# Performance work log

Hardware: AMD Instinct MI355X
Metric: run time of the kernel (lower is better)

## Reference

```python
import jax, jax.numpy as jnp
import numpy as np

B, T, H, L = 64, 512, 768, 9


def _crf_logZ(logits, transitions, seqlen):
    # forward algorithm; state freezes at t >= seqlen (tfa semantics)
    Tn = logits.shape[1]
    alpha0 = logits[:, 0]  # [B,L]
    valid = (jnp.arange(1, Tn)[None, :] < seqlen[:, None]).T  # [T-1,B]
    xs = (jnp.swapaxes(logits[:, 1:], 0, 1), valid)

    def step(alpha, inp):
        logit_t, v = inp
        new = jax.nn.logsumexp(alpha[:, :, None] + transitions[None], axis=1) + logit_t
        return jnp.where(v[:, None], new, alpha), None

    alphaT, _ = jax.lax.scan(step, alpha0, xs)
    return jax.nn.logsumexp(alphaT, axis=1)  # [B]


def _crf_score(logits, transitions, label, seqlen):
    Tn = logits.shape[1]
    seqmask = (jnp.arange(Tn)[None, :] < seqlen[:, None]).astype(logits.dtype)  # [B,T]
    unary = jnp.take_along_axis(logits, label[..., None], axis=2)[..., 0]
    unary = jnp.sum(unary * seqmask, axis=1)
    trans = transitions[label[:, :-1], label[:, 1:]]
    trans = jnp.sum(trans * seqmask[:, 1:], axis=1)
    return unary + trans  # [B]


def _viterbi(logits, transitions, seqlen):
    Tn, Ln = logits.shape[1], logits.shape[2]
    alpha0 = logits[:, 0]
    valid = (jnp.arange(1, Tn)[None, :] < seqlen[:, None]).T  # [T-1,B]
    xs = (jnp.swapaxes(logits[:, 1:], 0, 1), valid)
    idL = jnp.arange(Ln, dtype=jnp.int32)

    def step(alpha, inp):
        logit_t, v = inp
        scores = alpha[:, :, None] + transitions[None]  # [B,L,L]
        new = jnp.max(scores, axis=1) + logit_t
        bp = jnp.argmax(scores, axis=1).astype(jnp.int32)  # [B,L]
        alpha = jnp.where(v[:, None], new, alpha)
        bp = jnp.where(v[:, None], bp, idL[None, :])  # identity bp on padded steps
        return alpha, bp

    alphaT, bps = jax.lax.scan(step, alpha0, xs)  # bps: [T-1,B,L]
    last = jnp.argmax(alphaT, axis=1).astype(jnp.int32)  # [B]

    def back(tag, bp):
        prev = jnp.take_along_axis(bp, tag[:, None], axis=1)[:, 0]
        return prev, tag

    first, rest = jax.lax.scan(back, last, bps, reverse=True)
    tags = jnp.concatenate([first[None], rest], axis=0)  # [T,B]
    return jnp.swapaxes(tags, 0, 1)  # [B,T]


def setup_inputs() -> dict:
    key = jax.random.key(0)
    k = jax.random.split(key, 6)
    x = jax.random.normal(k[0], (B, T, H), dtype=jnp.float32)
    W = jax.random.truncated_normal(k[1], -2.0, 2.0, (H, L), dtype=jnp.float32) * 0.02
    b = jnp.zeros((L,), dtype=jnp.float32)
    lim = float(np.sqrt(6.0 / (L + L)))  # glorot_uniform
    transitions = jax.random.uniform(k[2], (L, L), dtype=jnp.float32, minval=-lim, maxval=lim)
    label = jax.random.randint(k[3], (B, T), 0, L, dtype=jnp.int32)
    seqlen = jax.random.randint(k[4], (B,), 1, T + 1, dtype=jnp.int32)
    mask = jnp.arange(T)[None, :] < seqlen[:, None]
    return {"x": x, "W": W, "b": b, "transitions": transitions, "label": label, "seqlen": seqlen, "mask": mask}


def reference(x, W, b, transitions, label, seqlen, mask):
    logits = jnp.einsum('bth,hl->btl', x, W) + b  # dense_ner
    ll = _crf_score(logits, transitions, label, seqlen) - _crf_logZ(logits, transitions, seqlen)
    loss = jnp.mean(-ll)
    vit = _viterbi(logits, transitions, seqlen)
    seqmask = (jnp.arange(logits.shape[1])[None, :] < seqlen[:, None]).astype(jnp.float32)
    accuracy = jnp.sum((vit == label).astype(jnp.float32) * seqmask) / jnp.sum(seqlen.astype(jnp.float32))
    tp = jnp.sum(((label > 0) & (vit == label)).astype(jnp.float32))
    tn = jnp.sum(((label > 0) & (vit != label)).astype(jnp.float32))
    fp = jnp.sum((mask & (label == 0) & (vit > 0)).astype(jnp.float32))
    return vit, tp, tn, fp, loss, accuracy
```

## Files before the change

### kernel.cpp

```cpp
#include <hip/hip_runtime.h>
#include <stdint.h>
#include <math.h>

#define NB 64
#define BT 512
#define NH 768
#define NL 9
#define PBT 528
#define PADW 772

__device__ __forceinline__ float rlane(float v, int i) {
    return __int_as_float(__builtin_amdgcn_readlane(__float_as_int(v), i));
}

template<int CTRL, int RM>
__device__ __forceinline__ float dppadd(float v) {
    const int t = __builtin_amdgcn_update_dpp(0, __float_as_int(v), CTRL, RM, 0xf, true);
    return v + __int_as_float(t);
}

__device__ __forceinline__ float wave_sum_dpp(float v) {
    v = dppadd<0x111, 0xf>(v);
    v = dppadd<0x112, 0xf>(v);
    v = dppadd<0x114, 0xf>(v);
    v = dppadd<0x118, 0xf>(v);
    v = dppadd<0x142, 0xa>(v);
    v = dppadd<0x143, 0xc>(v);
    return rlane(v, 63);
}

__global__ __launch_bounds__(256, 2) void gemm_kernel(
    const float* __restrict__ x, const float* __restrict__ W,
    const float* __restrict__ bias, float* __restrict__ logits)
{
    __shared__ float wT[NL * PADW];

    const int tid  = threadIdx.x;
    const int lane = tid & 63;

    for (int i = tid; i < NH * NL; i += 256) {
        const int h = i / NL, l = i - h * NL;
        wT[l * PADW + h] = W[i];
    }
    __syncthreads();

    float wr[3][NL][4];
#pragma unroll
    for (int k = 0; k < 3; ++k)
#pragma unroll
        for (int l = 0; l < NL; ++l) {
            const float4 w4 = *(const float4*)&wT[l * PADW + k * 256 + lane * 4];
            wr[k][l][0] = w4.x; wr[k][l][1] = w4.y;
            wr[k][l][2] = w4.z; wr[k][l][3] = w4.w;
        }
    const float bj = bias[lane < NL ? lane : 0];

    const int gwave = (blockIdx.x * blockDim.x + tid) >> 6;
    const int nw    = (gridDim.x * blockDim.x) >> 6;
    const int nrows = NB * BT;
    int row = gwave;
    if (row >= nrows) return;

    const float4* xr = (const float4*)(x + (size_t)row * NH);
    float4 a0 = xr[lane], a1 = xr[64 + lane], a2 = xr[128 + lane];

    while (true) {
        const int nrow = row + nw;
        float4 b0, b1, b2;
        if (nrow < nrows) {
            const float4* xn = (const float4*)(x + (size_t)nrow * NH);
            b0 = xn[lane]; b1 = xn[64 + lane]; b2 = xn[128 + lane];
        }

        float acc[NL];
#pragma unroll
        for (int l = 0; l < NL; ++l) {
            float s = a0.x * wr[0][l][0];
            s = fmaf(a0.y, wr[0][l][1], s);
            s = fmaf(a0.z, wr[0][l][2], s);
            s = fmaf(a0.w, wr[0][l][3], s);
            s = fmaf(a1.x, wr[1][l][0], s);
            s = fmaf(a1.y, wr[1][l][1], s);
            s = fmaf(a1.z, wr[1][l][2], s);
            s = fmaf(a1.w, wr[1][l][3], s);
            s = fmaf(a2.x, wr[2][l][0], s);
            s = fmaf(a2.y, wr[2][l][1], s);
            s = fmaf(a2.z, wr[2][l][2], s);
            s = fmaf(a2.w, wr[2][l][3], s);
            acc[l] = s;
        }
        float sum[NL];
#pragma unroll
        for (int l = 0; l < NL; ++l) sum[l] = wave_sum_dpp(acc[l]);
        float outv = sum[0];
#pragma unroll
        for (int l = 1; l < NL; ++l) outv = (lane == l) ? sum[l] : outv;
        if (lane < NL) logits[(size_t)row * NL + lane] = outv + bj;

        row = nrow;
        if (row >= nrows) break;
        a0 = b0; a1 = b1; a2 = b2;
    }
}

__global__ __launch_bounds__(256) void crf_kernel(
    const float* __restrict__ logits, const float* __restrict__ trans,
    const int* __restrict__ label, const int* __restrict__ seqlen,
    float* __restrict__ vit_out, float* __restrict__ stats)
{
    __shared__ __align__(16) float lg_lds[PBT * NL];
    __shared__ float    val_lds[BT * NL];
    __shared__ float    trans_lds[NL * NL];
    __shared__ uint8_t  bp_lds[(BT - 1) * NL];
    __shared__ uint64_t packed_lds[BT - 1];
    __shared__ uint8_t  vit_lds[BT];
    __shared__ float    xw[4][4];

    const int b    = blockIdx.x;
    const int tid  = threadIdx.x;
    const int lane = tid & 63;
    const int wv   = tid >> 6;
    const int sl   = seqlen[b];
    const float* lg  = logits + (size_t)b * BT * NL;
    const int*   lab = label + (size_t)b * BT;

    {
        const float4* src = (const float4*)lg;
        float4* dst = (float4*)lg_lds;
        for (int idx = tid; idx < BT * NL / 4; idx += 256) dst[idx] = src[idx];
        for (int idx = BT * NL + tid; idx < PBT * NL; idx += 256) lg_lds[idx] = 0.f;
        if (tid < NL * NL) trans_lds[tid] = trans[tid];
    }
    __syncthreads();

    if (wv == 0) {
        const int j = lane < NL ? lane : 0;
        float E[NL];
#pragma unroll
        for (int i = 0; i < NL; ++i) E[i] = __expf(trans_lds[i * NL + j]) * 0.125f;
        float A = __expf(lg_lds[j]);
        int lc = 0;
        for (int tb = 1; tb < BT + 8; tb += 8) {
            float P[8];
#pragma unroll
            for (int s = 0; s < 8; ++s) P[s] = __expf(lg_lds[(tb + s) * NL + j]);
#pragma unroll
            for (int s = 0; s < 8; ++s) {
                const int t = tb + s;
                const float r0 = rlane(A, 0), r1 = rlane(A, 1), r2 = rlane(A, 2),
                            r3 = rlane(A, 3), r4 = rlane(A, 4), r5 = rlane(A, 5),
                            r6 = rlane(A, 6), r7 = rlane(A, 7), r8 = rlane(A, 8);
                float p0 = r0 * E[0]; p0 = fmaf(r1, E[1], p0); p0 = fmaf(r2, E[2], p0);
                float p1 = r3 * E[3]; p1 = fmaf(r4, E[4], p1); p1 = fmaf(r5, E[5], p1);
                float p2 = r6 * E[6]; p2 = fmaf(r7, E[7], p2); p2 = fmaf(r8, E[8], p2);
                const float An = ((p0 + p1) + p2) * P[s];
                A = (t < sl) ? An : A;
            }
            const float m = fmaxf(fmaxf(
                fmaxf(fmaxf(rlane(A, 0), rlane(A, 1)), fmaxf(rlane(A, 2), rlane(A, 3))),
                fmaxf(fmaxf(rlane(A, 4), rlane(A, 5)), fmaxf(rlane(A, 6), rlane(A, 7)))),
                rlane(A, 8));
            const int ex = (int)((__float_as_uint(m) >> 23) & 0xFFu) - 126;
            const float sc = __uint_as_float((uint32_t)(127 - ex) << 23);
            A *= sc;
            lc += ex;
        }
        const float sum = ((rlane(A, 0) + rlane(A, 1)) + (rlane(A, 2) + rlane(A, 3))) +
                          ((rlane(A, 4) + rlane(A, 5)) + (rlane(A, 6) + rlane(A, 7))) +
                          rlane(A, 8);
        const float logZ = logf(sum) +
            ((float)lc + 3.0f * (float)(sl - 1)) * 0.6931471805599453f;
        if (lane == 0) stats[b * 8 + 1] = logZ;
    } else if (wv == 1) {
        const int j = lane < NL ? lane : 0;
        float tc[NL];
#pragma unroll
        for (int i = 0; i < NL; ++i) tc[i] = trans_lds[i * NL + j];
        float v = lg_lds[j];
        if (lane < NL) val_lds[j] = v;
        for (int tb = 1; tb < BT + 8; tb += 8) {
            float lv[8];
#pragma unroll
            for (int s = 0; s < 8; ++s) lv[s] = lg_lds[(tb + s) * NL + j];
#pragma unroll
            for (int s = 0; s < 8; ++s) {
                const int t = tb + s;
                const float r0 = rlane(v, 0), r1 = rlane(v, 1), r2 = rlane(v, 2),
                            r3 = rlane(v, 3), r4 = rlane(v, 4), r5 = rlane(v, 5),
                            r6 = rlane(v, 6), r7 = rlane(v, 7), r8 = rlane(v, 8);
                const float c0 = r0 + tc[0], c1 = r1 + tc[1], c2 = r2 + tc[2],
                            c3 = r3 + tc[3], c4 = r4 + tc[4], c5 = r5 + tc[5],
                            c6 = r6 + tc[6], c7 = r7 + tc[7], c8 = r8 + tc[8];
                const float m = fmaxf(fmaxf(fmaxf(fmaxf(c0, c1), c2),
                                            fmaxf(fmaxf(c3, c4), c5)),
                                      fmaxf(fmaxf(c6, c7), c8));
                const float nv = m + lv[s];
                v = (t < sl) ? nv : v;
                if (lane < NL && t < BT) val_lds[t * NL + lane] = v;
            }
        }
        const float r0 = rlane(v, 0), r1 = rlane(v, 1), r2 = rlane(v, 2),
                    r3 = rlane(v, 3), r4 = rlane(v, 4), r5 = rlane(v, 5),
                    r6 = rlane(v, 6), r7 = rlane(v, 7), r8 = rlane(v, 8);
        const float m = fmaxf(fmaxf(fmaxf(fmaxf(r0, r1), r2),
                                    fmaxf(fmaxf(r3, r4), r5)),
                              fmaxf(fmaxf(r6, r7), r8));
        const int last = (r0 == m) ? 0 : (r1 == m) ? 1 : (r2 == m) ? 2 :
                         (r3 == m) ? 3 : (r4 == m) ? 4 : (r5 == m) ? 5 :
                         (r6 == m) ? 6 : (r7 == m) ? 7 : 8;
        if (lane == 0) vit_lds[BT - 1] = (uint8_t)last;
    } else if (wv == 2) {
        float s = 0.f;
        for (int t = lane; t < BT; t += 64) {
            const int lb = lab[t];
            if (t < sl) {
                s += lg_lds[t * NL + lb];
                if (t >= 1) s += trans_lds[lab[t - 1] * NL + lb];
            }
        }
#pragma unroll
        for (int off = 32; off >= 1; off >>= 1) s += __shfl_xor(s, off, 64);
        if (lane == 0) stats[b * 8 + 0] = s;
    }
    __syncthreads();

    for (int idx = tid; idx < (BT - 1) * NL; idx += 256) {
        const int tm1 = idx / NL;
        const int jj  = idx - tm1 * NL;
        const int t   = tm1 + 1;
        int bi;
        if (t >= sl) bi = jj;
        else {
            float best = val_lds[tm1 * NL] + trans_lds[jj];
            bi = 0;
#pragma unroll
            for (int i = 1; i < NL; ++i) {
                const float c = val_lds[tm1 * NL + i] + trans_lds[i * NL + jj];
                if (c > best) { best = c; bi = i; }
            }
        }
        bp_lds[idx] = (uint8_t)bi;
    }
    __syncthreads();

    for (int r = tid; r < BT - 1; r += 256) {
        uint64_t p = 0;
#pragma unroll
        for (int i = 0; i < NL; ++i)
            p |= (uint64_t)bp_lds[r * NL + i] << (4 * i);
        packed_lds[r] = p;
    }
    __syncthreads();

    if (tid == 0) {
        int tag = vit_lds[BT - 1];
        for (int t = BT - 2; t >= 0; --t) {
            const uint64_t row = packed_lds[t];
            tag = (int)((row >> (4 * tag)) & 15u);
            vit_lds[t] = (uint8_t)tag;
        }
    }
    __syncthreads();

    float accv = 0.f, tpv = 0.f, tnv = 0.f, fpv = 0.f;
    for (int t = tid; t < BT; t += 256) {
        const int tg = vit_lds[t];
        const int lb = lab[t];
        const bool msk = t < sl;
        vit_out[(size_t)b * BT + t] = (float)tg;
        if (msk && tg == lb) accv += 1.f;
        if (lb > 0 && tg == lb) tpv += 1.f;
        if (lb > 0 && tg != lb) tnv += 1.f;
        if (msk && lb == 0 && tg > 0) fpv += 1.f;
    }
#pragma unroll
    for (int off = 32; off >= 1; off >>= 1) {
        accv += __shfl_xor(accv, off, 64);
        tpv  += __shfl_xor(tpv,  off, 64);
        tnv  += __shfl_xor(tnv,  off, 64);
        fpv  += __shfl_xor(fpv,  off, 64);
    }
    if (lane == 0) { xw[0][wv] = accv; xw[1][wv] = tpv; xw[2][wv] = tnv; xw[3][wv] = fpv; }
    __syncthreads();
    if (tid == 0) {
        stats[b * 8 + 2] = xw[0][0] + xw[0][1] + xw[0][2] + xw[0][3];
        stats[b * 8 + 3] = xw[1][0] + xw[1][1] + xw[1][2] + xw[1][3];
        stats[b * 8 + 4] = xw[2][0] + xw[2][1] + xw[2][2] + xw[2][3];
        stats[b * 8 + 5] = xw[3][0] + xw[3][1] + xw[3][2] + xw[3][3];
    }
}

__global__ __launch_bounds__(64) void finalize_kernel(
    const float* __restrict__ stats, const int* __restrict__ seqlen,
    float* __restrict__ out)
{
    const int lane = threadIdx.x;
    float score = stats[lane * 8 + 0];
    float logZ  = stats[lane * 8 + 1];
    float accv  = stats[lane * 8 + 2];
    float tpv   = stats[lane * 8 + 3];
    float tnv   = stats[lane * 8 + 4];
    float fpv   = stats[lane * 8 + 5];
    float nll   = logZ - score;
    float slf   = (float)seqlen[lane];
#pragma unroll
    for (int off = 32; off >= 1; off >>= 1) {
        nll  += __shfl_xor(nll,  off, 64);
        accv += __shfl_xor(accv, off, 64);
        tpv  += __shfl_xor(tpv,  off, 64);
        tnv  += __shfl_xor(tnv,  off, 64);
        fpv  += __shfl_xor(fpv,  off, 64);
        slf  += __shfl_xor(slf,  off, 64);
    }
    if (lane == 0) {
        out[NB * BT + 0] = tpv;
        out[NB * BT + 1] = tnv;
        out[NB * BT + 2] = fpv;
        out[NB * BT + 3] = nll / (float)NB;
        out[NB * BT + 4] = accv / slf;
    }
}

extern "C" void kernel_launch(void* const* d_in, const int* in_sizes, int n_in,
                              void* d_out, int out_size, void* d_ws, size_t ws_size,
                              hipStream_t stream)
{
    const float* x      = (const float*)d_in[0];
    const float* W      = (const float*)d_in[1];
    const float* bias   = (const float*)d_in[2];
    const float* trans  = (const float*)d_in[3];
    const int*   label  = (const int*)d_in[4];
    const int*   seqlen = (const int*)d_in[5];

    float* out    = (float*)d_out;
    float* logits = (float*)d_ws;
    float* stats  = logits + (size_t)NB * BT * NL;

    gemm_kernel<<<512, 256, 0, stream>>>(x, W, bias, logits);
    crf_kernel<<<NB, 256, 0, stream>>>(logits, trans, label, seqlen, out, stats);
    finalize_kernel<<<1, 64, 0, stream>>>(stats, seqlen, out);
}
```

Measured before the change: 212.7 us.

## Pack 8 sequences per CRF block, fuse Viterbi backpointers into forward scan

The CRF kernel now runs 8 batch rows per 1024-thread block. Waves 0-7 run the forward logZ recursion and later a wave-parallel backtrace that uses readlane over packed backpointers. Waves 8-15 run Viterbi, computing the argmax backpointers inline so the separate backpointer pass and the val_lds buffer are no longer needed. Logits are read straight from global memory with one-block-ahead register prefetch instead of being staged in LDS, and the GEMM prefetches two rows ahead. The CRF launch drops to 8 blocks, which gives fewer CUs in exchange for lower per-sequence overhead. The score computation moves onto the waves that also do Viterbi.

```diff
diff --git a/kernel.cpp b/kernel.cpp
--- a/kernel.cpp
+++ b/kernel.cpp
@@ -6,11 +6,15 @@
 #define BT 512
 #define NH 768
 #define NL 9
-#define PBT 528
 #define PADW 772
+#define BPB 8
+#define BPROW 16
 
 __device__ __forceinline__ float rlane(float v, int i) {
     return __int_as_float(__builtin_amdgcn_readlane(__float_as_int(v), i));
+}
+__device__ __forceinline__ uint32_t rlane_u(uint32_t v, int i) {
+    return (uint32_t)__builtin_amdgcn_readlane((int)v, i);
 }
 
 template<int CTRL, int RM>
@@ -64,12 +68,19 @@
     const float4* xr = (const float4*)(x + (size_t)row * NH);
     float4 a0 = xr[lane], a1 = xr[64 + lane], a2 = xr[128 + lane];
 
+    int r1 = row + nw;
+    float4 b0{}, b1{}, b2{};
+    if (r1 < nrows) {
+        const float4* xn = (const float4*)(x + (size_t)r1 * NH);
+        b0 = xn[lane]; b1 = xn[64 + lane]; b2 = xn[128 + lane];
+    }
+
     while (true) {
-        const int nrow = row + nw;
-        float4 b0, b1, b2;
-        if (nrow < nrows) {
-            const float4* xn = (const float4*)(x + (size_t)nrow * NH);
-            b0 = xn[lane]; b1 = xn[64 + lane]; b2 = xn[128 + lane];
+        const int r2 = r1 + nw;
+        float4 c0{}, c1{}, c2{};
+        if (r2 < nrows) {
+            const float4* xn = (const float4*)(x + (size_t)r2 * NH);
+            c0 = xn[lane]; c1 = xn[64 + lane]; c2 = xn[128 + lane];
         }
 
         float acc[NL];
@@ -97,53 +108,50 @@
         for (int l = 1; l < NL; ++l) outv = (lane == l) ? sum[l] : outv;
         if (lane < NL) logits[(size_t)row * NL + lane] = outv + bj;
 
-        row = nrow;
-        if (row >= nrows) break;
+        if (r1 >= nrows) break;
         a0 = b0; a1 = b1; a2 = b2;
-    }
-}
-
-__global__ __launch_bounds__(256) void crf_kernel(
+        b0 = c0; b1 = c1; b2 = c2;
+        row = r1; r1 = r2;
+    }
+}
+
+__global__ __launch_bounds__(1024) void crf_kernel(
     const float* __restrict__ logits, const float* __restrict__ trans,
     const int* __restrict__ label, const int* __restrict__ seqlen,
     float* __restrict__ vit_out, float* __restrict__ stats)
 {
-    __shared__ __align__(16) float lg_lds[PBT * NL];
-    __shared__ float    val_lds[BT * NL];
-    __shared__ float    trans_lds[NL * NL];
-    __shared__ uint8_t  bp_lds[(BT - 1) * NL];
-    __shared__ uint64_t packed_lds[BT - 1];
-    __shared__ uint8_t  vit_lds[BT];
-    __shared__ float    xw[4][4];
-
-    const int b    = blockIdx.x;
+    __shared__ uint8_t  bp_lds[BPB * (BT - 1) * BPROW];
+    __shared__ uint64_t packed_lds[BPB * (BT - 1)];
+    __shared__ uint8_t  vit_lds[BPB * BT];
+
     const int tid  = threadIdx.x;
     const int lane = tid & 63;
     const int wv   = tid >> 6;
+    const int w    = wv & 7;
+    const int b    = blockIdx.x * BPB + w;
     const int sl   = seqlen[b];
     const float* lg  = logits + (size_t)b * BT * NL;
     const int*   lab = label + (size_t)b * BT;
-
-    {
-        const float4* src = (const float4*)lg;
-        float4* dst = (float4*)lg_lds;
-        for (int idx = tid; idx < BT * NL / 4; idx += 256) dst[idx] = src[idx];
-        for (int idx = BT * NL + tid; idx < PBT * NL; idx += 256) lg_lds[idx] = 0.f;
-        if (tid < NL * NL) trans_lds[tid] = trans[tid];
-    }
-    __syncthreads();
-
-    if (wv == 0) {
-        const int j = lane < NL ? lane : 0;
+    const int j = lane < NL ? lane : 0;
+
+    if (wv < 8) {
         float E[NL];
 #pragma unroll
-        for (int i = 0; i < NL; ++i) E[i] = __expf(trans_lds[i * NL + j]) * 0.125f;
-        float A = __expf(lg_lds[j]);
+        for (int i = 0; i < NL; ++i) E[i] = __expf(trans[i * NL + j]) * 0.125f;
+        float A = __expf(lg[j]);
         int lc = 0;
+        float cur[8], nxt[8];
+#pragma unroll
+        for (int s = 0; s < 8; ++s) cur[s] = lg[(1 + s) * NL + j];
         for (int tb = 1; tb < BT + 8; tb += 8) {
+#pragma unroll
+            for (int s = 0; s < 8; ++s) {
+                int tt = tb + 8 + s; if (tt > BT - 1) tt = BT - 1;
+                nxt[s] = lg[tt * NL + j];
+            }
             float P[8];
 #pragma unroll
-            for (int s = 0; s < 8; ++s) P[s] = __expf(lg_lds[(tb + s) * NL + j]);
+            for (int s = 0; s < 8; ++s) P[s] = __expf(cur[s]);
 #pragma unroll
             for (int s = 0; s < 8; ++s) {
                 const int t = tb + s;
@@ -156,14 +164,16 @@
                 const float An = ((p0 + p1) + p2) * P[s];
                 A = (t < sl) ? An : A;
             }
-            const float m = fmaxf(fmaxf(
-                fmaxf(fmaxf(rlane(A, 0), rlane(A, 1)), fmaxf(rlane(A, 2), rlane(A, 3))),
-                fmaxf(fmaxf(rlane(A, 4), rlane(A, 5)), fmaxf(rlane(A, 6), rlane(A, 7)))),
-                rlane(A, 8));
+            const float m = fmaxf(
+                fmaxf(fmaxf(fmaxf(rlane(A, 0), rlane(A, 1)), rlane(A, 2)),
+                      fmaxf(fmaxf(rlane(A, 3), rlane(A, 4)), rlane(A, 5))),
+                fmaxf(fmaxf(rlane(A, 6), rlane(A, 7)), rlane(A, 8)));
             const int ex = (int)((__float_as_uint(m) >> 23) & 0xFFu) - 126;
             const float sc = __uint_as_float((uint32_t)(127 - ex) << 23);
             A *= sc;
             lc += ex;
+#pragma unroll
+            for (int s = 0; s < 8; ++s) cur[s] = nxt[s];
         }
         const float sum = ((rlane(A, 0) + rlane(A, 1)) + (rlane(A, 2) + rlane(A, 3))) +
                           ((rlane(A, 4) + rlane(A, 5)) + (rlane(A, 6) + rlane(A, 7))) +
@@ -171,17 +181,20 @@
         const float logZ = logf(sum) +
             ((float)lc + 3.0f * (float)(sl - 1)) * 0.6931471805599453f;
         if (lane == 0) stats[b * 8 + 1] = logZ;
-    } else if (wv == 1) {
-        const int j = lane < NL ? lane : 0;
+    } else {
         float tc[NL];
 #pragma unroll
-        for (int i = 0; i < NL; ++i) tc[i] = trans_lds[i * NL + j];
-        float v = lg_lds[j];
-        if (lane < NL) val_lds[j] = v;
+        for (int i = 0; i < NL; ++i) tc[i] = trans[i * NL + j];
+        float v = lg[j];
+        float cur[8], nxt[8];
+#pragma unroll
+        for (int s = 0; s < 8; ++s) cur[s] = lg[(1 + s) * NL + j];
         for (int tb = 1; tb < BT + 8; tb += 8) {
-            float lv[8];
-#pragma unroll
-            for (int s = 0; s < 8; ++s) lv[s] = lg_lds[(tb + s) * NL + j];
+#pragma unroll
+            for (int s = 0; s < 8; ++s) {
+                int tt = tb + 8 + s; if (tt > BT - 1) tt = BT - 1;
+                nxt[s] = lg[tt * NL + j];
+            }
 #pragma unroll
             for (int s = 0; s < 8; ++s) {
                 const int t = tb + s;
@@ -191,31 +204,84 @@
                 const float c0 = r0 + tc[0], c1 = r1 + tc[1], c2 = r2 + tc[2],
                             c3 = r3 + tc[3], c4 = r4 + tc[4], c5 = r5 + tc[5],
                             c6 = r6 + tc[6], c7 = r7 + tc[7], c8 = r8 + tc[8];
-                const float m = fmaxf(fmaxf(fmaxf(fmaxf(c0, c1), c2),
-                                            fmaxf(fmaxf(c3, c4), c5)),
-                                      fmaxf(fmaxf(c6, c7), c8));
-                const float nv = m + lv[s];
+                const float m = fmaxf(
+                    fmaxf(fmaxf(fmaxf(c0, c1), c2), fmaxf(fmaxf(c3, c4), c5)),
+                    fmaxf(fmaxf(c6, c7), c8));
+                const float nv = m + cur[s];
                 v = (t < sl) ? nv : v;
-                if (lane < NL && t < BT) val_lds[t * NL + lane] = v;
-            }
+                int bi = 8;
+                bi = (c7 == m) ? 7 : bi;
+                bi = (c6 == m) ? 6 : bi;
+                bi = (c5 == m) ? 5 : bi;
+                bi = (c4 == m) ? 4 : bi;
+                bi = (c3 == m) ? 3 : bi;
+                bi = (c2 == m) ? 2 : bi;
+                bi = (c1 == m) ? 1 : bi;
+                bi = (c0 == m) ? 0 : bi;
+                bi = (t < sl) ? bi : j;
+                if (lane < NL && t < BT)
+                    bp_lds[(w * (BT - 1) + (t - 1)) * BPROW + lane] = (uint8_t)bi;
+            }
+#pragma unroll
+            for (int s = 0; s < 8; ++s) cur[s] = nxt[s];
         }
         const float r0 = rlane(v, 0), r1 = rlane(v, 1), r2 = rlane(v, 2),
                     r3 = rlane(v, 3), r4 = rlane(v, 4), r5 = rlane(v, 5),
                     r6 = rlane(v, 6), r7 = rlane(v, 7), r8 = rlane(v, 8);
-        const float m = fmaxf(fmaxf(fmaxf(fmaxf(r0, r1), r2),
-                                    fmaxf(fmaxf(r3, r4), r5)),
-                              fmaxf(fmaxf(r6, r7), r8));
+        const float m = fmaxf(
+            fmaxf(fmaxf(fmaxf(r0, r1), r2), fmaxf(fmaxf(r3, r4), r5)),
+            fmaxf(fmaxf(r6, r7), r8));
         const int last = (r0 == m) ? 0 : (r1 == m) ? 1 : (r2 == m) ? 2 :
                          (r3 == m) ? 3 : (r4 == m) ? 4 : (r5 == m) ? 5 :
                          (r6 == m) ? 6 : (r7 == m) ? 7 : 8;
-        if (lane == 0) vit_lds[BT - 1] = (uint8_t)last;
-    } else if (wv == 2) {
+        if (lane == 0) vit_lds[w * BT + BT - 1] = (uint8_t)last;
+    }
+    __syncthreads();
+
+    for (int idx = tid; idx < BPB * (BT - 1); idx += 1024) {
+        const int base = idx * BPROW;
+        uint64_t p = 0;
+#pragma unroll
+        for (int i = 0; i < NL; ++i)
+            p |= (uint64_t)bp_lds[base + i] << (4 * i);
+        packed_lds[idx] = p;
+    }
+    __syncthreads();
+
+    if (wv < 8) {
+        uint32_t plo[8], phi[8];
+#pragma unroll
+        for (int r = 0; r < 8; ++r) {
+            const int t = r * 64 + lane;
+            uint64_t val = 0;
+            if (t < BT - 1) val = packed_lds[w * (BT - 1) + t];
+            plo[r] = (uint32_t)val;
+            phi[r] = (uint32_t)(val >> 32);
+        }
+        int tag = vit_lds[w * BT + BT - 1];
+#pragma unroll
+        for (int r = 7; r >= 0; --r) {
+            const int lhi = (r == 7) ? 62 : 63;
+#pragma unroll 4
+            for (int l = lhi; l >= 0; --l) {
+                const uint32_t lo = rlane_u(plo[r], l);
+                const uint32_t hi = rlane_u(phi[r], l);
+                const uint32_t ww = (tag & 8) ? hi : lo;
+                tag = (int)((ww >> ((4 * tag) & 31)) & 15u);
+                if (lane == 0) vit_lds[w * BT + r * 64 + l] = (uint8_t)tag;
+            }
+        }
+    } else {
+        int labv[8];
+#pragma unroll
+        for (int k = 0; k < 8; ++k) labv[k] = lab[lane + 64 * k];
         float s = 0.f;
-        for (int t = lane; t < BT; t += 64) {
-            const int lb = lab[t];
+#pragma unroll
+        for (int k = 0; k < 8; ++k) {
+            const int t = lane + 64 * k;
             if (t < sl) {
-                s += lg_lds[t * NL + lb];
-                if (t >= 1) s += trans_lds[lab[t - 1] * NL + lb];
+                s += lg[t * NL + labv[k]];
+                if (t >= 1) s += trans[lab[t - 1] * NL + labv[k]];
             }
         }
 #pragma unroll
@@ -224,69 +290,33 @@
     }
     __syncthreads();
 
-    for (int idx = tid; idx < (BT - 1) * NL; idx += 256) {
-        const int tm1 = idx / NL;
-        const int jj  = idx - tm1 * NL;
-        const int t   = tm1 + 1;
-        int bi;
-        if (t >= sl) bi = jj;
-        else {
-            float best = val_lds[tm1 * NL] + trans_lds[jj];
-            bi = 0;
-#pragma unroll
-            for (int i = 1; i < NL; ++i) {
-                const float c = val_lds[tm1 * NL + i] + trans_lds[i * NL + jj];
-                if (c > best) { best = c; bi = i; }
-            }
-        }
-        bp_lds[idx] = (uint8_t)bi;
-    }
-    __syncthreads();
-
-    for (int r = tid; r < BT - 1; r += 256) {
-        uint64_t p = 0;
-#pragma unroll
-        for (int i = 0; i < NL; ++i)
-            p |= (uint64_t)bp_lds[r * NL + i] << (4 * i);
-        packed_lds[r] = p;
-    }
-    __syncthreads();
-
-    if (tid == 0) {
-        int tag = vit_lds[BT - 1];
-        for (int t = BT - 2; t >= 0; --t) {
-            const uint64_t row = packed_lds[t];
-            tag = (int)((row >> (4 * tag)) & 15u);
-            vit_lds[t] = (uint8_t)tag;
-        }
-    }
-    __syncthreads();
-
-    float accv = 0.f, tpv = 0.f, tnv = 0.f, fpv = 0.f;
-    for (int t = tid; t < BT; t += 256) {
-        const int tg = vit_lds[t];
-        const int lb = lab[t];
-        const bool msk = t < sl;
-        vit_out[(size_t)b * BT + t] = (float)tg;
-        if (msk && tg == lb) accv += 1.f;
-        if (lb > 0 && tg == lb) tpv += 1.f;
-        if (lb > 0 && tg != lb) tnv += 1.f;
-        if (msk && lb == 0 && tg > 0) fpv += 1.f;
-    }
-#pragma unroll
-    for (int off = 32; off >= 1; off >>= 1) {
-        accv += __shfl_xor(accv, off, 64);
-        tpv  += __shfl_xor(tpv,  off, 64);
-        tnv  += __shfl_xor(tnv,  off, 64);
-        fpv  += __shfl_xor(fpv,  off, 64);
-    }
-    if (lane == 0) { xw[0][wv] = accv; xw[1][wv] = tpv; xw[2][wv] = tnv; xw[3][wv] = fpv; }
-    __syncthreads();
-    if (tid == 0) {
-        stats[b * 8 + 2] = xw[0][0] + xw[0][1] + xw[0][2] + xw[0][3];
-        stats[b * 8 + 3] = xw[1][0] + xw[1][1] + xw[1][2] + xw[1][3];
-        stats[b * 8 + 4] = xw[2][0] + xw[2][1] + xw[2][2] + xw[2][3];
-        stats[b * 8 + 5] = xw[3][0] + xw[3][1] + xw[3][2] + xw[3][3];
+    if (wv < 8) {
+        float accv = 0.f, tpv = 0.f, tnv = 0.f, fpv = 0.f;
+#pragma unroll
+        for (int k = 0; k < 8; ++k) {
+            const int t = lane + 64 * k;
+            const int tg = vit_lds[w * BT + t];
+            const int lb = lab[t];
+            const bool msk = t < sl;
+            vit_out[(size_t)b * BT + t] = (float)tg;
+            if (msk && tg == lb) accv += 1.f;
+            if (lb > 0 && tg == lb) tpv += 1.f;
+            if (lb > 0 && tg != lb) tnv += 1.f;
+            if (msk && lb == 0 && tg > 0) fpv += 1.f;
+        }
+#pragma unroll
+        for (int off = 32; off >= 1; off >>= 1) {
+            accv += __shfl_xor(accv, off, 64);
+            tpv  += __shfl_xor(tpv,  off, 64);
+            tnv  += __shfl_xor(tnv,  off, 64);
+            fpv  += __shfl_xor(fpv,  off, 64);
+        }
+        if (lane == 0) {
+            stats[b * 8 + 2] = accv;
+            stats[b * 8 + 3] = tpv;
+            stats[b * 8 + 4] = tnv;
+            stats[b * 8 + 5] = fpv;
+        }
     }
 }
 
@@ -337,6 +367,6 @@
     float* stats  = logits + (size_t)NB * BT * NL;
 
     gemm_kernel<<<512, 256, 0, stream>>>(x, W, bias, logits);
-    crf_kernel<<<NB, 256, 0, stream>>>(logits, trans, label, seqlen, out, stats);
+    crf_kernel<<<NB / BPB, 1024, 0, stream>>>(logits, trans, label, seqlen, out, stats);
     finalize_kernel<<<1, 64, 0, stream>>>(stats, seqlen, out);
 }
```

Measured after the change: 336.3 us. 58.1% more time.

## Deepen gemm prefetch to four rows per stage with double buffering

Applied to the files above, without the earlier changes.

The grid-stride GEMM loop now runs a fixed schedule. Each wave handles 16 rows in four groups of four, and the next group's x loads are issued while the current group is computed. This keeps more global loads in flight per wave to hide HBM latency in a bandwidth-bound GEMV. It hardcodes 2048 waves (the launch grid must match) and raises register use; the launch_bounds minimum-blocks hint is dropped to allow that.

```diff
diff --git a/kernel.cpp b/kernel.cpp
--- a/kernel.cpp
+++ b/kernel.cpp
@@ -8,6 +8,7 @@
 #define NL 9
 #define PBT 528
 #define PADW 772
+#define NWAVE 2048
 
 __device__ __forceinline__ float rlane(float v, int i) {
     return __int_as_float(__builtin_amdgcn_readlane(__float_as_int(v), i));
@@ -29,7 +30,7 @@
     return rlane(v, 63);
 }
 
-__global__ __launch_bounds__(256, 2) void gemm_kernel(
+__global__ __launch_bounds__(256) void gemm_kernel(
     const float* __restrict__ x, const float* __restrict__ W,
     const float* __restrict__ bias, float* __restrict__ logits)
 {
@@ -55,51 +56,61 @@
         }
     const float bj = bias[lane < NL ? lane : 0];
 
-    const int gwave = (blockIdx.x * blockDim.x + tid) >> 6;
-    const int nw    = (gridDim.x * blockDim.x) >> 6;
-    const int nrows = NB * BT;
-    int row = gwave;
-    if (row >= nrows) return;
-
-    const float4* xr = (const float4*)(x + (size_t)row * NH);
-    float4 a0 = xr[lane], a1 = xr[64 + lane], a2 = xr[128 + lane];
-
-    while (true) {
-        const int nrow = row + nw;
-        float4 b0, b1, b2;
-        if (nrow < nrows) {
-            const float4* xn = (const float4*)(x + (size_t)nrow * NH);
-            b0 = xn[lane]; b1 = xn[64 + lane]; b2 = xn[128 + lane];
-        }
-
-        float acc[NL];
-#pragma unroll
-        for (int l = 0; l < NL; ++l) {
-            float s = a0.x * wr[0][l][0];
-            s = fmaf(a0.y, wr[0][l][1], s);
-            s = fmaf(a0.z, wr[0][l][2], s);
-            s = fmaf(a0.w, wr[0][l][3], s);
-            s = fmaf(a1.x, wr[1][l][0], s);
-            s = fmaf(a1.y, wr[1][l][1], s);
-            s = fmaf(a1.z, wr[1][l][2], s);
-            s = fmaf(a1.w, wr[1][l][3], s);
-            s = fmaf(a2.x, wr[2][l][0], s);
-            s = fmaf(a2.y, wr[2][l][1], s);
-            s = fmaf(a2.z, wr[2][l][2], s);
-            s = fmaf(a2.w, wr[2][l][3], s);
-            acc[l] = s;
-        }
-        float sum[NL];
-#pragma unroll
-        for (int l = 0; l < NL; ++l) sum[l] = wave_sum_dpp(acc[l]);
-        float outv = sum[0];
-#pragma unroll
-        for (int l = 1; l < NL; ++l) outv = (lane == l) ? sum[l] : outv;
-        if (lane < NL) logits[(size_t)row * NL + lane] = outv + bj;
-
-        row = nrow;
-        if (row >= nrows) break;
-        a0 = b0; a1 = b1; a2 = b2;
+    const int gw = (blockIdx.x * blockDim.x + tid) >> 6;
+
+    float4 buf[2][4][3];
+#pragma unroll
+    for (int q = 0; q < 4; ++q) {
+        const float4* p = (const float4*)(x + (size_t)(gw + q * NWAVE) * NH);
+        buf[0][q][0] = p[lane];
+        buf[0][q][1] = p[64 + lane];
+        buf[0][q][2] = p[128 + lane];
+    }
+
+#pragma unroll
+    for (int grp = 0; grp < 4; ++grp) {
+        const int cb = grp & 1, nb = cb ^ 1;
+        if (grp < 3) {
+#pragma unroll
+            for (int q = 0; q < 4; ++q) {
+                const float4* p = (const float4*)(
+                    x + (size_t)(gw + ((grp + 1) * 4 + q) * NWAVE) * NH);
+                buf[nb][q][0] = p[lane];
+                buf[nb][q][1] = p[64 + lane];
+                buf[nb][q][2] = p[128 + lane];
+            }
+        }
+#pragma unroll
+        for (int q = 0; q < 4; ++q) {
+            const float4 a0 = buf[cb][q][0];
+            const float4 a1 = buf[cb][q][1];
+            const float4 a2 = buf[cb][q][2];
+            float acc[NL];
+#pragma unroll
+            for (int l = 0; l < NL; ++l) {
+                float s = a0.x * wr[0][l][0];
+                s = fmaf(a0.y, wr[0][l][1], s);
+                s = fmaf(a0.z, wr[0][l][2], s);
+                s = fmaf(a0.w, wr[0][l][3], s);
+                s = fmaf(a1.x, wr[1][l][0], s);
+                s = fmaf(a1.y, wr[1][l][1], s);
+                s = fmaf(a1.z, wr[1][l][2], s);
+                s = fmaf(a1.w, wr[1][l][3], s);
+                s = fmaf(a2.x, wr[2][l][0], s);
+                s = fmaf(a2.y, wr[2][l][1], s);
+                s = fmaf(a2.z, wr[2][l][2], s);
+                s = fmaf(a2.w, wr[2][l][3], s);
+                acc[l] = s;
+            }
+            float sum[NL];
+#pragma unroll
+            for (int l = 0; l < NL; ++l) sum[l] = wave_sum_dpp(acc[l]);
+            float outv = sum[0];
+#pragma unroll
+            for (int l = 1; l < NL; ++l) outv = (lane == l) ? sum[l] : outv;
+            const int row = gw + (grp * 4 + q) * NWAVE;
+            if (lane < NL) logits[(size_t)row * NL + lane] = outv + bj;
+        }
     }
 }
 
```

Result: slower. 217.6 us (+2.3%).

## Process two sequences per CRF block to interleave independent recurrences

Applied to the files above, without the earlier changes.

Each CRF block now handles two batch rows, and the forward and Viterbi waves advance two independent recurrence chains in the same loop. The goal is instruction-level parallelism that hides the readlane and FMA latency of the serial dependency chain. In exchange the grid shrinks to 32 blocks, so fewer CUs are used. LDS per block roughly doubles, and the backtrace runs on two waves in parallel.

```diff
diff --git a/kernel.cpp b/kernel.cpp
--- a/kernel.cpp
+++ b/kernel.cpp
@@ -8,6 +8,7 @@
 #define NL 9
 #define PBT 528
 #define PADW 772
+#define NBB 2
 
 __device__ __forceinline__ float rlane(float v, int i) {
     return __int_as_float(__builtin_amdgcn_readlane(__float_as_int(v), i));
@@ -108,185 +109,283 @@
     const int* __restrict__ label, const int* __restrict__ seqlen,
     float* __restrict__ vit_out, float* __restrict__ stats)
 {
-    __shared__ __align__(16) float lg_lds[PBT * NL];
-    __shared__ float    val_lds[BT * NL];
+    __shared__ __align__(16) float lg_lds[NBB][PBT * NL];
+    __shared__ float    val_lds[NBB][BT * NL];
     __shared__ float    trans_lds[NL * NL];
-    __shared__ uint8_t  bp_lds[(BT - 1) * NL];
-    __shared__ uint64_t packed_lds[BT - 1];
-    __shared__ uint8_t  vit_lds[BT];
+    __shared__ uint8_t  bp_lds[NBB][(BT - 1) * NL];
+    __shared__ uint64_t packed_lds[NBB][BT - 1];
+    __shared__ uint8_t  vit_lds[NBB][BT];
     __shared__ float    xw[4][4];
 
-    const int b    = blockIdx.x;
     const int tid  = threadIdx.x;
     const int lane = tid & 63;
     const int wv   = tid >> 6;
-    const int sl   = seqlen[b];
-    const float* lg  = logits + (size_t)b * BT * NL;
-    const int*   lab = label + (size_t)b * BT;
+    const int b0   = blockIdx.x * NBB;
+    const int sl0  = seqlen[b0];
+    const int sl1  = seqlen[b0 + 1];
+    const float* lg0 = logits + (size_t)b0 * BT * NL;
+    const float* lg1 = lg0 + BT * NL;
+    const int j = lane < NL ? lane : 0;
 
     {
-        const float4* src = (const float4*)lg;
-        float4* dst = (float4*)lg_lds;
-        for (int idx = tid; idx < BT * NL / 4; idx += 256) dst[idx] = src[idx];
-        for (int idx = BT * NL + tid; idx < PBT * NL; idx += 256) lg_lds[idx] = 0.f;
+        const float4* s0 = (const float4*)lg0;
+        const float4* s1 = (const float4*)lg1;
+        float4* d0 = (float4*)&lg_lds[0][0];
+        float4* d1 = (float4*)&lg_lds[1][0];
+        for (int idx = tid; idx < BT * NL / 4; idx += 256) {
+            d0[idx] = s0[idx];
+            d1[idx] = s1[idx];
+        }
+        for (int idx = BT * NL + tid; idx < PBT * NL; idx += 256) {
+            lg_lds[0][idx] = 0.f;
+            lg_lds[1][idx] = 0.f;
+        }
         if (tid < NL * NL) trans_lds[tid] = trans[tid];
     }
     __syncthreads();
 
     if (wv == 0) {
-        const int j = lane < NL ? lane : 0;
         float E[NL];
 #pragma unroll
         for (int i = 0; i < NL; ++i) E[i] = __expf(trans_lds[i * NL + j]) * 0.125f;
-        float A = __expf(lg_lds[j]);
-        int lc = 0;
+        float A0 = __expf(lg_lds[0][j]);
+        float A1 = __expf(lg_lds[1][j]);
+        int lc0 = 0, lc1 = 0;
         for (int tb = 1; tb < BT + 8; tb += 8) {
-            float P[8];
-#pragma unroll
-            for (int s = 0; s < 8; ++s) P[s] = __expf(lg_lds[(tb + s) * NL + j]);
+            float P0[8], P1[8];
+#pragma unroll
+            for (int s = 0; s < 8; ++s) {
+                P0[s] = __expf(lg_lds[0][(tb + s) * NL + j]);
+                P1[s] = __expf(lg_lds[1][(tb + s) * NL + j]);
+            }
 #pragma unroll
             for (int s = 0; s < 8; ++s) {
                 const int t = tb + s;
-                const float r0 = rlane(A, 0), r1 = rlane(A, 1), r2 = rlane(A, 2),
-                            r3 = rlane(A, 3), r4 = rlane(A, 4), r5 = rlane(A, 5),
-                            r6 = rlane(A, 6), r7 = rlane(A, 7), r8 = rlane(A, 8);
-                float p0 = r0 * E[0]; p0 = fmaf(r1, E[1], p0); p0 = fmaf(r2, E[2], p0);
-                float p1 = r3 * E[3]; p1 = fmaf(r4, E[4], p1); p1 = fmaf(r5, E[5], p1);
-                float p2 = r6 * E[6]; p2 = fmaf(r7, E[7], p2); p2 = fmaf(r8, E[8], p2);
-                const float An = ((p0 + p1) + p2) * P[s];
-                A = (t < sl) ? An : A;
-            }
-            const float m = fmaxf(fmaxf(
-                fmaxf(fmaxf(rlane(A, 0), rlane(A, 1)), fmaxf(rlane(A, 2), rlane(A, 3))),
-                fmaxf(fmaxf(rlane(A, 4), rlane(A, 5)), fmaxf(rlane(A, 6), rlane(A, 7)))),
-                rlane(A, 8));
-            const int ex = (int)((__float_as_uint(m) >> 23) & 0xFFu) - 126;
-            const float sc = __uint_as_float((uint32_t)(127 - ex) << 23);
-            A *= sc;
-            lc += ex;
-        }
-        const float sum = ((rlane(A, 0) + rlane(A, 1)) + (rlane(A, 2) + rlane(A, 3))) +
-                          ((rlane(A, 4) + rlane(A, 5)) + (rlane(A, 6) + rlane(A, 7))) +
-                          rlane(A, 8);
-        const float logZ = logf(sum) +
-            ((float)lc + 3.0f * (float)(sl - 1)) * 0.6931471805599453f;
-        if (lane == 0) stats[b * 8 + 1] = logZ;
+                {
+                    const float r0 = rlane(A0, 0), r1 = rlane(A0, 1), r2 = rlane(A0, 2),
+                                r3 = rlane(A0, 3), r4 = rlane(A0, 4), r5 = rlane(A0, 5),
+                                r6 = rlane(A0, 6), r7 = rlane(A0, 7), r8 = rlane(A0, 8);
+                    float p0 = r0 * E[0]; p0 = fmaf(r1, E[1], p0); p0 = fmaf(r2, E[2], p0);
+                    float p1 = r3 * E[3]; p1 = fmaf(r4, E[4], p1); p1 = fmaf(r5, E[5], p1);
+                    float p2 = r6 * E[6]; p2 = fmaf(r7, E[7], p2); p2 = fmaf(r8, E[8], p2);
+                    const float An = ((p0 + p1) + p2) * P0[s];
+                    A0 = (t < sl0) ? An : A0;
+                }
+                {
+                    const float r0 = rlane(A1, 0), r1 = rlane(A1, 1), r2 = rlane(A1, 2),
+                                r3 = rlane(A1, 3), r4 = rlane(A1, 4), r5 = rlane(A1, 5),
+                                r6 = rlane(A1, 6), r7 = rlane(A1, 7), r8 = rlane(A1, 8);
+                    float p0 = r0 * E[0]; p0 = fmaf(r1, E[1], p0); p0 = fmaf(r2, E[2], p0);
+                    float p1 = r3 * E[3]; p1 = fmaf(r4, E[4], p1); p1 = fmaf(r5, E[5], p1);
+                    float p2 = r6 * E[6]; p2 = fmaf(r7, E[7], p2); p2 = fmaf(r8, E[8], p2);
+                    const float An = ((p0 + p1) + p2) * P1[s];
+                    A1 = (t < sl1) ? An : A1;
+                }
+            }
+            {
+                const float m = fmaxf(fmaxf(
+                    fmaxf(fmaxf(rlane(A0, 0), rlane(A0, 1)), fmaxf(rlane(A0, 2), rlane(A0, 3))),
+                    fmaxf(fmaxf(rlane(A0, 4), rlane(A0, 5)), fmaxf(rlane(A0, 6), rlane(A0, 7)))),
+                    rlane(A0, 8));
+                const int ex = (int)((__float_as_uint(m) >> 23) & 0xFFu) - 126;
+                const float sc = __uint_as_float((uint32_t)(127 - ex) << 23);
+                A0 *= sc;
+                lc0 += ex;
+            }
+            {
+                const float m = fmaxf(fmaxf(
+                    fmaxf(fmaxf(rlane(A1, 0), rlane(A1, 1)), fmaxf(rlane(A1, 2), rlane(A1, 3))),
+                    fmaxf(fmaxf(rlane(A1, 4), rlane(A1, 5)), fmaxf(rlane(A1, 6), rlane(A1, 7)))),
+                    rlane(A1, 8));
+                const int ex = (int)((__float_as_uint(m) >> 23) & 0xFFu) - 126;
+                const float sc = __uint_as_float((uint32_t)(127 - ex) << 23);
+                A1 *= sc;
+                lc1 += ex;
+            }
+        }
+        const float sum0 = ((rlane(A0, 0) + rlane(A0, 1)) + (rlane(A0, 2) + rlane(A0, 3))) +
+                           ((rlane(A0, 4) + rlane(A0, 5)) + (rlane(A0, 6) + rlane(A0, 7))) +
+                           rlane(A0, 8);
+        const float sum1 = ((rlane(A1, 0) + rlane(A1, 1)) + (rlane(A1, 2) + rlane(A1, 3))) +
+                           ((rlane(A1, 4) + rlane(A1, 5)) + (rlane(A1, 6) + rlane(A1, 7))) +
+                           rlane(A1, 8);
+        const float logZ0 = logf(sum0) +
+            ((float)lc0 + 3.0f * (float)(sl0 - 1)) * 0.6931471805599453f;
+        const float logZ1 = logf(sum1) +
+            ((float)lc1 + 3.0f * (float)(sl1 - 1)) * 0.6931471805599453f;
+        if (lane == 0) {
+            stats[b0 * 8 + 1]       = logZ0;
+            stats[(b0 + 1) * 8 + 1] = logZ1;
+        }
     } else if (wv == 1) {
-        const int j = lane < NL ? lane : 0;
         float tc[NL];
 #pragma unroll
         for (int i = 0; i < NL; ++i) tc[i] = trans_lds[i * NL + j];
-        float v = lg_lds[j];
-        if (lane < NL) val_lds[j] = v;
+        float v0 = lg_lds[0][j];
+        float v1 = lg_lds[1][j];
+        if (lane < NL) {
+            val_lds[0][j] = v0;
+            val_lds[1][j] = v1;
+        }
         for (int tb = 1; tb < BT + 8; tb += 8) {
-            float lv[8];
-#pragma unroll
-            for (int s = 0; s < 8; ++s) lv[s] = lg_lds[(tb + s) * NL + j];
+            float lv0[8], lv1[8];
+#pragma unroll
+            for (int s = 0; s < 8; ++s) {
+                lv0[s] = lg_lds[0][(tb + s) * NL + j];
+                lv1[s] = lg_lds[1][(tb + s) * NL + j];
+            }
 #pragma unroll
             for (int s = 0; s < 8; ++s) {
                 const int t = tb + s;
-                const float r0 = rlane(v, 0), r1 = rlane(v, 1), r2 = rlane(v, 2),
-                            r3 = rlane(v, 3), r4 = rlane(v, 4), r5 = rlane(v, 5),
-                            r6 = rlane(v, 6), r7 = rlane(v, 7), r8 = rlane(v, 8);
-                const float c0 = r0 + tc[0], c1 = r1 + tc[1], c2 = r2 + tc[2],
-                            c3 = r3 + tc[3], c4 = r4 + tc[4], c5 = r5 + tc[5],
-                            c6 = r6 + tc[6], c7 = r7 + tc[7], c8 = r8 + tc[8];
-                const float m = fmaxf(fmaxf(fmaxf(fmaxf(c0, c1), c2),
-                                            fmaxf(fmaxf(c3, c4), c5)),
-                                      fmaxf(fmaxf(c6, c7), c8));
-                const float nv = m + lv[s];
-                v = (t < sl) ? nv : v;
-                if (lane < NL && t < BT) val_lds[t * NL + lane] = v;
-            }
-        }
-        const float r0 = rlane(v, 0), r1 = rlane(v, 1), r2 = rlane(v, 2),
-                    r3 = rlane(v, 3), r4 = rlane(v, 4), r5 = rlane(v, 5),
-                    r6 = rlane(v, 6), r7 = rlane(v, 7), r8 = rlane(v, 8);
-        const float m = fmaxf(fmaxf(fmaxf(fmaxf(r0, r1), r2),
-                                    fmaxf(fmaxf(r3, r4), r5)),
-                              fmaxf(fmaxf(r6, r7), r8));
-        const int last = (r0 == m) ? 0 : (r1 == m) ? 1 : (r2 == m) ? 2 :
-                         (r3 == m) ? 3 : (r4 == m) ? 4 : (r5 == m) ? 5 :
-                         (r6 == m) ? 6 : (r7 == m) ? 7 : 8;
-        if (lane == 0) vit_lds[BT - 1] = (uint8_t)last;
-    } else if (wv == 2) {
+                {
+                    const float r0 = rlane(v0, 0), r1 = rlane(v0, 1), r2 = rlane(v0, 2),
+                                r3 = rlane(v0, 3), r4 = rlane(v0, 4), r5 = rlane(v0, 5),
+                                r6 = rlane(v0, 6), r7 = rlane(v0, 7), r8 = rlane(v0, 8);
+                    const float c0 = r0 + tc[0], c1 = r1 + tc[1], c2 = r2 + tc[2],
+                                c3 = r3 + tc[3], c4 = r4 + tc[4], c5 = r5 + tc[5],
+                                c6 = r6 + tc[6], c7 = r7 + tc[7], c8 = r8 + tc[8];
+                    const float m = fmaxf(fmaxf(fmaxf(fmaxf(c0, c1), c2),
+                                                fmaxf(fmaxf(c3, c4), c5)),
+                                          fmaxf(fmaxf(c6, c7), c8));
+                    const float nv = m + lv0[s];
+                    v0 = (t < sl0) ? nv : v0;
+                }
+                {
+                    const float r0 = rlane(v1, 0), r1 = rlane(v1, 1), r2 = rlane(v1, 2),
+                                r3 = rlane(v1, 3), r4 = rlane(v1, 4), r5 = rlane(v1, 5),
+                                r6 = rlane(v1, 6), r7 = rlane(v1, 7), r8 = rlane(v1, 8);
+                    const float c0 = r0 + tc[0], c1 = r1 + tc[1], c2 = r2 + tc[2],
+                                c3 = r3 + tc[3], c4 = r4 + tc[4], c5 = r5 + tc[5],
+                                c6 = r6 + tc[6], c7 = r7 + tc[7], c8 = r8 + tc[8];
+                    const float m = fmaxf(fmaxf(fmaxf(fmaxf(c0, c1), c2),
+                                                fmaxf(fmaxf(c3, c4), c5)),
+                                          fmaxf(fmaxf(c6, c7), c8));
+                    const float nv = m + lv1[s];
+                    v1 = (t < sl1) ? nv : v1;
+                }
+                if (lane < NL && t < BT) {
+                    val_lds[0][t * NL + lane] = v0;
+                    val_lds[1][t * NL + lane] = v1;
+                }
+            }
+        }
+        {
+            const float r0 = rlane(v0, 0), r1 = rlane(v0, 1), r2 = rlane(v0, 2),
+                        r3 = rlane(v0, 3), r4 = rlane(v0, 4), r5 = rlane(v0, 5),
+                        r6 = rlane(v0, 6), r7 = rlane(v0, 7), r8 = rlane(v0, 8);
+            const float m = fmaxf(fmaxf(fmaxf(fmaxf(r0, r1), r2),
+                                        fmaxf(fmaxf(r3, r4), r5)),
+                                  fmaxf(fmaxf(r6, r7), r8));
+            const int last = (r0 == m) ? 0 : (r1 == m) ? 1 : (r2 == m) ? 2 :
+                             (r3 == m) ? 3 : (r4 == m) ? 4 : (r5 == m) ? 5 :
+                             (r6 == m) ? 6 : (r7 == m) ? 7 : 8;
+            if (lane == 0) vit_lds[0][BT - 1] = (uint8_t)last;
+        }
+        {
+            const float r0 = rlane(v1, 0), r1 = rlane(v1, 1), r2 = rlane(v1, 2),
+                        r3 = rlane(v1, 3), r4 = rlane(v1, 4), r5 = rlane(v1, 5),
+                        r6 = rlane(v1, 6), r7 = rlane(v1, 7), r8 = rlane(v1, 8);
+            const float m = fmaxf(fmaxf(fmaxf(fmaxf(r0, r1), r2),
+                                        fmaxf(fmaxf(r3, r4), r5)),
+                                  fmaxf(fmaxf(r6, r7), r8));
+            const int last = (r0 == m) ? 0 : (r1 == m) ? 1 : (r2 == m) ? 2 :
+                             (r3 == m) ? 3 : (r4 == m) ? 4 : (r5 == m) ? 5 :
+                             (r6 == m) ? 6 : (r7 == m) ? 7 : 8;
+            if (lane == 0) vit_lds[1][BT - 1] = (uint8_t)last;
+        }
+    } else {
+        const int bb = wv - 2;
+        const int sl = bb ? sl1 : sl0;
+        const int* lab = label + (size_t)(b0 + bb) * BT;
         float s = 0.f;
         for (int t = lane; t < BT; t += 64) {
             const int lb = lab[t];
             if (t < sl) {
-                s += lg_lds[t * NL + lb];
+                s += lg_lds[bb][t * NL + lb];
                 if (t >= 1) s += trans_lds[lab[t - 1] * NL + lb];
             }
         }
 #pragma unroll
         for (int off = 32; off >= 1; off >>= 1) s += __shfl_xor(s, off, 64);
-        if (lane == 0) stats[b * 8 + 0] = s;
-    }
-    __syncthreads();
-
-    for (int idx = tid; idx < (BT - 1) * NL; idx += 256) {
-        const int tm1 = idx / NL;
-        const int jj  = idx - tm1 * NL;
+        if (lane == 0) stats[(b0 + bb) * 8 + 0] = s;
+    }
+    __syncthreads();
+
+    for (int idx = tid; idx < NBB * (BT - 1) * NL; idx += 256) {
+        const int bb  = idx / ((BT - 1) * NL);
+        const int rem = idx - bb * (BT - 1) * NL;
+        const int tm1 = rem / NL;
+        const int jj  = rem - tm1 * NL;
         const int t   = tm1 + 1;
+        const int sl  = bb ? sl1 : sl0;
         int bi;
         if (t >= sl) bi = jj;
         else {
-            float best = val_lds[tm1 * NL] + trans_lds[jj];
+            float best = val_lds[bb][tm1 * NL] + trans_lds[jj];
             bi = 0;
 #pragma unroll
             for (int i = 1; i < NL; ++i) {
-                const float c = val_lds[tm1 * NL + i] + trans_lds[i * NL + jj];
+                const float c = val_lds[bb][tm1 * NL + i] + trans_lds[i * NL + jj];
                 if (c > best) { best = c; bi = i; }
             }
         }
-        bp_lds[idx] = (uint8_t)bi;
-    }
-    __syncthreads();
-
-    for (int r = tid; r < BT - 1; r += 256) {
+        bp_lds[bb][rem] = (uint8_t)bi;
+    }
+    __syncthreads();
+
+    for (int r = tid; r < NBB * (BT - 1); r += 256) {
+        const int bb = r / (BT - 1);
+        const int rr = r - bb * (BT - 1);
         uint64_t p = 0;
 #pragma unroll
         for (int i = 0; i < NL; ++i)
-            p |= (uint64_t)bp_lds[r * NL + i] << (4 * i);
-        packed_lds[r] = p;
-    }
-    __syncthreads();
-
-    if (tid == 0) {
-        int tag = vit_lds[BT - 1];
+            p |= (uint64_t)bp_lds[bb][rr * NL + i] << (4 * i);
+        packed_lds[bb][rr] = p;
+    }
+    __syncthreads();
+
+    if (lane == 0 && wv < NBB) {
+        const int bb = wv;
+        int tag = vit_lds[bb][BT - 1];
         for (int t = BT - 2; t >= 0; --t) {
-            const uint64_t row = packed_lds[t];
+            const uint64_t row = packed_lds[bb][t];
             tag = (int)((row >> (4 * tag)) & 15u);
-            vit_lds[t] = (uint8_t)tag;
-        }
-    }
-    __syncthreads();
-
-    float accv = 0.f, tpv = 0.f, tnv = 0.f, fpv = 0.f;
-    for (int t = tid; t < BT; t += 256) {
-        const int tg = vit_lds[t];
-        const int lb = lab[t];
-        const bool msk = t < sl;
-        vit_out[(size_t)b * BT + t] = (float)tg;
-        if (msk && tg == lb) accv += 1.f;
-        if (lb > 0 && tg == lb) tpv += 1.f;
-        if (lb > 0 && tg != lb) tnv += 1.f;
-        if (msk && lb == 0 && tg > 0) fpv += 1.f;
-    }
-#pragma unroll
-    for (int off = 32; off >= 1; off >>= 1) {
-        accv += __shfl_xor(accv, off, 64);
-        tpv  += __shfl_xor(tpv,  off, 64);
-        tnv  += __shfl_xor(tnv,  off, 64);
-        fpv  += __shfl_xor(fpv,  off, 64);
-    }
-    if (lane == 0) { xw[0][wv] = accv; xw[1][wv] = tpv; xw[2][wv] = tnv; xw[3][wv] = fpv; }
-    __syncthreads();
-    if (tid == 0) {
-        stats[b * 8 + 2] = xw[0][0] + xw[0][1] + xw[0][2] + xw[0][3];
-        stats[b * 8 + 3] = xw[1][0] + xw[1][1] + xw[1][2] + xw[1][3];
-        stats[b * 8 + 4] = xw[2][0] + xw[2][1] + xw[2][2] + xw[2][3];
-        stats[b * 8 + 5] = xw[3][0] + xw[3][1] + xw[3][2] + xw[3][3];
+            vit_lds[bb][t] = (uint8_t)tag;
+        }
+    }
+    __syncthreads();
+
+    for (int bb = 0; bb < NBB; ++bb) {
+        const int b  = b0 + bb;
+        const int sl = bb ? sl1 : sl0;
+        const int* lab = label + (size_t)b * BT;
+        float accv = 0.f, tpv = 0.f, tnv = 0.f, fpv = 0.f;
+        for (int t = tid; t < BT; t += 256) {
+            const int tg = vit_lds[bb][t];
+            const int lb = lab[t];
+            const bool msk = t < sl;
+            vit_out[(size_t)b * BT + t] = (float)tg;
+            if (msk && tg == lb) accv += 1.f;
+            if (lb > 0 && tg == lb) tpv += 1.f;
+            if (lb > 0 && tg != lb) tnv += 1.f;
+            if (msk && lb == 0 && tg > 0) fpv += 1.f;
+        }
+#pragma unroll
+        for (int off = 32; off >= 1; off >>= 1) {
+            accv += __shfl_xor(accv, off, 64);
+            tpv  += __shfl_xor(tpv,  off, 64);
+            tnv  += __shfl_xor(tnv,  off, 64);
+            fpv  += __shfl_xor(fpv,  off, 64);
+        }
+        if (lane == 0) { xw[0][wv] = accv; xw[1][wv] = tpv; xw[2][wv] = tnv; xw[3][wv] = fpv; }
+        __syncthreads();
+        if (tid == 0) {
+            stats[b * 8 + 2] = xw[0][0] + xw[0][1] + xw[0][2] + xw[0][3];
+            stats[b * 8 + 3] = xw[1][0] + xw[1][1] + xw[1][2] + xw[1][3];
+            stats[b * 8 + 4] = xw[2][0] + xw[2][1] + xw[2][2] + xw[2][3];
+            stats[b * 8 + 5] = xw[3][0] + xw[3][1] + xw[3][2] + xw[3][3];
+        }
+        __syncthreads();
     }
 }
 
@@ -337,6 +436,6 @@
     float* stats  = logits + (size_t)NB * BT * NL;
 
     gemm_kernel<<<512, 256, 0, stream>>>(x, W, bias, logits);
-    crf_kernel<<<NB, 256, 0, stream>>>(logits, trans, label, seqlen, out, stats);
+    crf_kernel<<<NB / NBB, 256, 0, stream>>>(logits, trans, label, seqlen, out, stats);
     finalize_kernel<<<1, 64, 0, stream>>>(stats, seqlen, out);
 }
```

Measured after the change: 252.6 us. +18.8%, slower.
